# Performance work log

Hardware: AMD Instinct MI355X
Metric: run time of the kernel (lower is better)

## Reference

```python
import jax, jax.numpy as jnp
import numpy as np

B = 8192       # batch
HID = 1024     # hidden_dim
HEADS = 8      # head_count
OBS, ACT, N_AGENTS = 128, 32, 4
ENC_IN = N_AGENTS * OBS + ACT   # 544
DEC_IN = (N_AGENTS - 1) * ACT   # 96


def _linear(key, fan_in, fan_out):
    k1, k2 = jax.random.split(key)
    lim = 1.0 / np.sqrt(fan_in)
    W = jax.random.uniform(k1, (fan_in, fan_out), minval=-lim, maxval=lim, dtype=jnp.float32)
    b = jax.random.uniform(k2, (fan_out,), minval=-lim, maxval=lim, dtype=jnp.float32)
    return W, b


def setup_inputs() -> dict:
    key = jax.random.key(0)
    ks = jax.random.split(key, 10)
    s = jax.random.normal(ks[0], (B, N_AGENTS * OBS), dtype=jnp.float32)
    a = jax.random.normal(ks[1], (B, N_AGENTS * ACT), dtype=jnp.float32)
    W_enc_in, b_enc_in = _linear(ks[2], ENC_IN, HID)   # encoder_input_fc
    W_dec_in, b_dec_in = _linear(ks[3], DEC_IN, HID)   # decoder_input_fc
    W_eh, b_eh = _linear(ks[4], HID, HID)              # fc_encoder_input
    head_ks = jax.random.split(ks[5], HEADS)
    Wb = [_linear(k, HID, HID) for k in head_ks]       # fc_encoder_heads
    W_heads = jnp.stack([w for w, _ in Wb], axis=0)    # [H, HID, HID]
    b_heads = jnp.stack([b for _, b in Wb], axis=0)    # [H, HID]
    W_dh, b_dh = _linear(ks[6], HID, HID)              # fc_decoder_input
    W1, b1 = _linear(ks[7], HID, HID)                  # fc1
    W2, b2 = _linear(ks[8], HID, 1)                    # fc2
    return {"s": s, "a": a,
            "W_enc_in": W_enc_in, "b_enc_in": b_enc_in,
            "W_dec_in": W_dec_in, "b_dec_in": b_dec_in,
            "W_eh": W_eh, "b_eh": b_eh,
            "W_heads": W_heads, "b_heads": b_heads,
            "W_dh": W_dh, "b_dh": b_dh,
            "W1": W1, "b1": b1, "W2": W2, "b2": b2}


def reference(s, a, W_enc_in, b_enc_in, W_dec_in, b_dec_in, W_eh, b_eh,
              W_heads, b_heads, W_dh, b_dh, W1, b1, W2, b2):
    relu = jax.nn.relu
    # agent id = 0: own action is a[:, :ACT], others' actions are a[:, ACT:]
    enc_input = jnp.concatenate([s, a[:, :ACT]], axis=1) @ W_enc_in + b_enc_in   # [B, HID]
    dec_input = a[:, ACT:] @ W_dec_in + b_dec_in                                 # [B, HID]
    # Attention_ATT_2
    encoder_h = relu(enc_input @ W_eh + b_eh)                                    # [B, HID]
    encoder_heads = relu(jnp.einsum('bd,hde->hbe', encoder_h, W_heads)
                         + b_heads[:, None, :])                                  # [H, B, HID]
    decoder_H = relu(dec_input @ W_dh + b_dh)                                    # [B, HID]
    scores = jnp.einsum('hbd,bd->bh', encoder_heads, decoder_H)                  # [B, H]
    attn = jax.nn.softmax(scores, axis=1)                                        # [B, H]
    context = jnp.einsum('hbd,bh->bd', encoder_heads, attn)                      # [B, HID]
    x = relu(context @ W1 + b1)
    q = x @ W2 + b2                                                              # [B, 1]
    return q
```

## Files before the change

kernel.cpp:

```cpp
#include <hip/hip_runtime.h>
#include <hip/hip_bf16.h>
#include <hip/hip_fp16.h>

#define BATCH   8192
#define HID     1024
#define HEADS   8
#define BC      2048

typedef unsigned int  u32;
typedef unsigned short u16;
typedef __attribute__((ext_vector_type(8))) short bf16x8;
typedef __attribute__((ext_vector_type(4))) float f32x4;

__device__ __forceinline__ u32 pack_hi2(u32 u0, u32 u1) {
    return (u0 >> 16) | (u1 & 0xFFFF0000u);
}
__device__ __forceinline__ void split1(float x, u16& h, u16& l) {
    const u32 u = __float_as_uint(x);
    h = (u16)(u >> 16);
    const float r = x - __uint_as_float(u & 0xFFFF0000u);
    l = (u16)(__float_as_uint(r) >> 16);
}
__device__ __forceinline__ void splitA4(float4 v, uint2& hi, uint2& lo) {
    u32 u0 = __float_as_uint(v.x), u1 = __float_as_uint(v.y),
        u2 = __float_as_uint(v.z), u3 = __float_as_uint(v.w);
    float r0 = v.x - __uint_as_float(u0 & 0xFFFF0000u);
    float r1 = v.y - __uint_as_float(u1 & 0xFFFF0000u);
    float r2 = v.z - __uint_as_float(u2 & 0xFFFF0000u);
    float r3 = v.w - __uint_as_float(u3 & 0xFFFF0000u);
    hi.x = pack_hi2(u0, u1);
    hi.y = pack_hi2(u2, u3);
    lo.x = pack_hi2(__float_as_uint(r0), __float_as_uint(r1));
    lo.y = pack_hi2(__float_as_uint(r2), __float_as_uint(r3));
}

__device__ __forceinline__ void gld16(const u16* g, u16* l) {
    __builtin_amdgcn_global_load_lds(
        (const __attribute__((address_space(1))) u32*)g,
        (__attribute__((address_space(3))) u32*)l, 16, 0, 0);
}

struct WSplitArgs {
    const float* src[6];
    u16* hi[6];
    u16* lo[6];
};

__global__ __launch_bounds__(256) void split_weight_all(WSplitArgs args)
{
    const int z = blockIdx.z;
    int which, zz = 0;
    if (z < 3)       { which = z; }
    else if (z < 11) { which = 3; zz = z - 3; }
    else             { which = z - 7; }
    const int KT = (which == 4) ? 17 : (which == 5 ? 3 : 32);
    const int kt = blockIdx.x;
    if (kt >= KT) return;
    const int K = KT * 32;
    const long long zoff = (long long)zz * K * 1024;
    const float* W  = args.src[which] + zoff;
    u16* hi = args.hi[which] + zoff;
    u16* lo = args.lo[which] + zoff;

    const int n0  = blockIdx.y * 128;
    const int tid = threadIdx.x;
    const int k   = tid >> 3;
    const int ng  = (tid & 7) * 16;
    const float* src = W + (long long)(kt * 32 + k) * 1024 + n0 + ng;
    u16* dh = hi + ((long long)kt * 1024 + n0) * 32 + k;
    u16* dl = lo + ((long long)kt * 1024 + n0) * 32 + k;
#pragma unroll
    for (int t = 0; t < 4; t++) {
        const float4 v = *(const float4*)(src + t * 4);
        u16 h0, l0, h1, l1, h2, l2, h3, l3;
        split1(v.x, h0, l0); split1(v.y, h1, l1);
        split1(v.z, h2, l2); split1(v.w, h3, l3);
        const int nb = (ng + t * 4) * 32;
        dh[nb]      = h0; dl[nb]      = l0;
        dh[nb + 32] = h1; dl[nb + 32] = l1;
        dh[nb + 64] = h2; dl[nb + 64] = l2;
        dh[nb + 96] = h3; dl[nb + 96] = l3;
    }
}

#define PIPE_GEOM \
    const int tid  = threadIdx.x; \
    const int lane = tid & 63; \
    const int wv   = tid >> 6; \
    const int wm   = wv >> 1, wn = wv & 1; \
    const int fr   = lane & 15; \
    const int fq   = lane >> 4; \
    const int m0   = blockIdx.y * 256; \
    const int n0   = blockIdx.x * 128; \
    const int lro2 = (lane >> 2) * 32 + (((lane & 3) ^ ((lane >> 3) & 3)) * 8); \
    const int fqx2 = (fq ^ ((fr >> 1) & 3)) * 8; \
    const int wr   = wv * 16;

#define PSTAGE_HI(dst_, aoff_, boff_) { \
    u16* db_ = (dst_); \
    gld16(Ahp + (aoff_) + (long long)wr * 32 + lro2, db_ + wr * 32); \
    gld16(Ahp + (aoff_) + (long long)(128 + wr) * 32 + lro2, db_ + (128 + wr) * 32); \
    gld16(Bhp + (boff_) + (long long)wr * 32 + lro2, db_ + 16384 + wr * 32); }

#define PSTAGE_LO(dst_, aoff_, boff_) { \
    u16* db_ = (dst_); \
    gld16(Alp + (aoff_) + (long long)wr * 32 + lro2, db_ + 8192 + wr * 32); \
    gld16(Alp + (aoff_) + (long long)(128 + wr) * 32 + lro2, db_ + 8192 + (128 + wr) * 32); \
    gld16(Blp + (boff_) + (long long)wr * 32 + lro2, db_ + 20480 + wr * 32); }

#define PTILE(t_, STAGE0_, STAGE1_, TAILWAIT_) { \
    const u16* bufp = smem + ((t_) % 3) * 24576; \
    bf16x8 bh[4], bl[4], ah0[2], al0[2], ah1[2], al1[2]; \
    _Pragma("unroll") \
    for (int j = 0; j < 4; j++) { \
        const int off = (wn * 64 + j * 16 + fr) * 32 + fqx2; \
        bh[j] = *(const bf16x8*)(bufp + 16384 + off); \
        bl[j] = *(const bf16x8*)(bufp + 20480 + off); } \
    _Pragma("unroll") \
    for (int i = 0; i < 2; i++) { \
        const int off = (wm * 64 + i * 16 + fr) * 32 + fqx2; \
        ah0[i] = *(const bf16x8*)(bufp + off); \
        al0[i] = *(const bf16x8*)(bufp + 8192 + off); } \
    STAGE0_; \
    __builtin_amdgcn_s_barrier(); \
    __builtin_amdgcn_s_setprio(1); \
    _Pragma("unroll") \
    for (int i = 0; i < 2; i++) \
        _Pragma("unroll") \
        for (int j = 0; j < 4; j++) { \
            acc[i][j] = __builtin_amdgcn_mfma_f32_16x16x32_bf16(ah0[i], bh[j], acc[i][j], 0, 0, 0); \
            acc[i][j] = __builtin_amdgcn_mfma_f32_16x16x32_bf16(ah0[i], bl[j], acc[i][j], 0, 0, 0); \
            acc[i][j] = __builtin_amdgcn_mfma_f32_16x16x32_bf16(al0[i], bh[j], acc[i][j], 0, 0, 0); } \
    __builtin_amdgcn_s_setprio(0); \
    __builtin_amdgcn_s_barrier(); \
    __builtin_amdgcn_sched_barrier(0); \
    _Pragma("unroll") \
    for (int i = 0; i < 2; i++) { \
        const int off = (wm * 64 + (2 + i) * 16 + fr) * 32 + fqx2; \
        ah1[i] = *(const bf16x8*)(bufp + off); \
        al1[i] = *(const bf16x8*)(bufp + 8192 + off); } \
    STAGE1_; \
    __builtin_amdgcn_s_barrier(); \
    __builtin_amdgcn_s_setprio(1); \
    _Pragma("unroll") \
    for (int i = 0; i < 2; i++) \
        _Pragma("unroll") \
        for (int j = 0; j < 4; j++) { \
            acc[2 + i][j] = __builtin_amdgcn_mfma_f32_16x16x32_bf16(ah1[i], bh[j], acc[2 + i][j], 0, 0, 0); \
            acc[2 + i][j] = __builtin_amdgcn_mfma_f32_16x16x32_bf16(ah1[i], bl[j], acc[2 + i][j], 0, 0, 0); \
            acc[2 + i][j] = __builtin_amdgcn_mfma_f32_16x16x32_bf16(al1[i], bh[j], acc[2 + i][j], 0, 0, 0); } \
    __builtin_amdgcn_s_setprio(0); \
    TAILWAIT_; \
    __builtin_amdgcn_s_barrier(); \
    __builtin_amdgcn_sched_barrier(0); \
}

#define PIPE_LOOP \
    const int KT = K >> 5; \
    const long long astep = (long long)MA * 32; \
    const long long bstep = 32768; \
    const long long abase = ((long long)moff + m0) * 32; \
    const long long bbase = (long long)n0 * 32; \
    PSTAGE_HI(smem, abase, bbase); \
    PSTAGE_LO(smem, abase, bbase); \
    PSTAGE_HI(smem + 24576, abase + astep, bbase + bstep); \
    PSTAGE_LO(smem + 24576, abase + astep, bbase + bstep); \
    asm volatile("s_waitcnt vmcnt(6)" ::: "memory"); \
    __builtin_amdgcn_s_barrier(); \
    __builtin_amdgcn_sched_barrier(0); \
    for (int t = 0; t < KT - 2; t++) { \
        u16* dst2 = smem + ((t + 2) % 3) * 24576; \
        const long long a2 = abase + (long long)(t + 2) * astep; \
        const long long b2 = bbase + (long long)(t + 2) * bstep; \
        PTILE(t, PSTAGE_HI(dst2, a2, b2), PSTAGE_LO(dst2, a2, b2), \
              asm volatile("s_waitcnt vmcnt(6)" ::: "memory")); \
    } \
    PTILE(KT - 2, ((void)0), ((void)0), \
          asm volatile("s_waitcnt vmcnt(0)" ::: "memory")); \
    PTILE(KT - 1, ((void)0), ((void)0), ((void)0));

template <int RELU, int OUTP>
__global__ __launch_bounds__(512) void gemm_fast(
    const u16* __restrict__ Ahp, const u16* __restrict__ Alp, int MA, int moff,
    const u16* __restrict__ Bhp, const u16* __restrict__ Blp,
    const float* __restrict__ bias,
    float* __restrict__ Cf,
    u16* __restrict__ Chp, u16* __restrict__ Clp, int MC,
    int K)
{
    __shared__ alignas(16) u16 smem[3 * 24576];
    PIPE_GEOM

    f32x4 acc[4][4];
#pragma unroll
    for (int i = 0; i < 4; i++)
#pragma unroll
        for (int j = 0; j < 4; j++) acc[i][j] = 0;

    PIPE_LOOP

#pragma unroll
    for (int j = 0; j < 4; j++) {
        const int n = n0 + wn * 64 + j * 16 + fr;
        const float bb = bias[n];
#pragma unroll
        for (int i = 0; i < 4; i++) {
#pragma unroll
            for (int r = 0; r < 4; r++) {
                const int m = m0 + wm * 64 + i * 16 + fq * 4 + r;
                float v = acc[i][j][r] + bb;
                if (RELU) v = fmaxf(v, 0.0f);
                if (OUTP) {
                    u16 h, l;
                    split1(v, h, l);
                    const long long d = ((long long)(n >> 5) * MC + moff + m) * 32 + (n & 31);
                    Chp[d] = h;
                    Clp[d] = l;
                } else {
                    Cf[(long long)m * 1024 + n] = v;
                }
            }
        }
    }
}

__global__ __launch_bounds__(512) void heads_kernel(
    const u16* __restrict__ Ahp, const u16* __restrict__ Alp, int MA, int moff,
    const u16* __restrict__ Whp, const u16* __restrict__ Wlp,
    const float* __restrict__ b_heads,
    const float* __restrict__ decH,
    __half* __restrict__ headsb,
    float* __restrict__ scoresp)
{
    __shared__ alignas(16) u16 smem[3 * 24576];
    __shared__ float scred[2][256];
    PIPE_GEOM
    const int h = blockIdx.z;
    const u16* Bhp = Whp + (long long)h * 1048576;
    const u16* Blp = Wlp + (long long)h * 1048576;
    const float* bias = b_heads + h * 1024;
    const int K = 1024;

    f32x4 acc[4][4];
#pragma unroll
    for (int i = 0; i < 4; i++)
#pragma unroll
        for (int j = 0; j < 4; j++) acc[i][j] = 0;

    PIPE_LOOP

    float part[4][4];
#pragma unroll
    for (int i = 0; i < 4; i++)
#pragma unroll
        for (int r = 0; r < 4; r++) part[i][r] = 0.0f;

#pragma unroll
    for (int j = 0; j < 4; j++) {
        const int n = n0 + wn * 64 + j * 16 + fr;
        const float bb = bias[n];
#pragma unroll
        for (int i = 0; i < 4; i++) {
#pragma unroll
            for (int r = 0; r < 4; r++) {
                const int b_loc = m0 + wm * 64 + i * 16 + fq * 4 + r;
                const float v = fmaxf(acc[i][j][r] + bb, 0.0f);
                headsb[((long long)b_loc * HEADS + h) * 1024 + n] = __float2half(v);
                part[i][r] = fmaf(v, decH[(long long)b_loc * 1024 + n], part[i][r]);
            }
        }
    }
#pragma unroll
    for (int off = 1; off < 16; off <<= 1)
#pragma unroll
        for (int i = 0; i < 4; i++)
#pragma unroll
            for (int r = 0; r < 4; r++)
                part[i][r] += __shfl_xor(part[i][r], off, 64);

    if (fr == 0) {
#pragma unroll
        for (int i = 0; i < 4; i++)
#pragma unroll
            for (int r = 0; r < 4; r++)
                scred[wn][wm * 64 + i * 16 + fq * 4 + r] = part[i][r];
    }
    __syncthreads();
    if (tid < 256) {
        const float sv = scred[0][tid] + scred[1][tid];
        scoresp[(long long)(h * 8 + blockIdx.x) * BC + m0 + tid] = sv;
    }
}

template <int RELU>
__global__ __launch_bounds__(256) void gemm_cvt(
    const float* __restrict__ src1, int lda1, int kofs1,
    const float* __restrict__ src2, int lda2, int ksplit,
    const u16* __restrict__ Bhp, const u16* __restrict__ Blp,
    const float* __restrict__ bias,
    u16* __restrict__ Chp, u16* __restrict__ Clp, int MC,
    int K)
{
    __shared__ alignas(16) u16 Ah[4096], Al[4096], Bh[4096], Bl[4096];
    const int tid  = threadIdx.x;
    const int lane = tid & 63;
    const int wv   = tid >> 6;
    const int wm   = wv >> 1, wn = wv & 1;
    const int fr   = lane & 15;
    const int fq   = lane >> 4;
    const int m0   = blockIdx.y * 128;
    const int n0   = blockIdx.x * 128;
    const int fqx  = (fq ^ (fr & 3)) * 8;
    const int lro  = (lane >> 2) * 32 + (((lane & 3) ^ ((lane >> 2) & 3)) * 8);
    const int br0  = wv * 16;
    const int br1  = 64 + wv * 16;
    const int ar   = tid >> 3;
    const int akq  = tid & 7;
    const int awoff = (((akq >> 1) ^ (ar & 3)) * 8) + (akq & 1) * 4;

    f32x4 acc[4][4];
#pragma unroll
    for (int i = 0; i < 4; i++)
#pragma unroll
        for (int j = 0; j < 4; j++) acc[i][j] = 0;

    const int KT = K >> 5;
    for (int kt = 0; kt < KT; kt++) {
        const int k0 = kt * 32;
        const float* srcp; int ldk, kc;
        if (k0 < ksplit) { srcp = src1; ldk = lda1; kc = k0 + kofs1; }
        else             { srcp = src2; ldk = lda2; kc = k0 - ksplit; }

        const u16* Bg  = Bhp + ((long long)kt * 1024 + n0) * 32;
        const u16* Bg2 = Blp + ((long long)kt * 1024 + n0) * 32;
        gld16(Bg  + br0 * 32 + lro, &Bh[br0 * 32]);
        gld16(Bg  + br1 * 32 + lro, &Bh[br1 * 32]);
        gld16(Bg2 + br0 * 32 + lro, &Bl[br0 * 32]);
        gld16(Bg2 + br1 * 32 + lro, &Bl[br1 * 32]);

#pragma unroll
        for (int it = 0; it < 4; it++) {
            const int row = ar + it * 32;
            const float4 v = *(const float4*)(srcp + (long long)(m0 + row) * ldk + kc + akq * 4);
            uint2 hi, lo;
            splitA4(v, hi, lo);
            *(uint2*)&Ah[row * 32 + awoff] = hi;
            *(uint2*)&Al[row * 32 + awoff] = lo;
        }
        __syncthreads();

        bf16x8 ah[4], al[4], bh[4], bl[4];
#pragma unroll
        for (int i = 0; i < 4; i++) {
            const int off = (wm * 64 + i * 16 + fr) * 32 + fqx;
            ah[i] = *(const bf16x8*)&Ah[off];
            al[i] = *(const bf16x8*)&Al[off];
        }
#pragma unroll
        for (int j = 0; j < 4; j++) {
            const int off = (wn * 64 + j * 16 + fr) * 32 + fqx;
            bh[j] = *(const bf16x8*)&Bh[off];
            bl[j] = *(const bf16x8*)&Bl[off];
        }
#pragma unroll
        for (int i = 0; i < 4; i++)
#pragma unroll
            for (int j = 0; j < 4; j++) {
                acc[i][j] = __builtin_amdgcn_mfma_f32_16x16x32_bf16(ah[i], bh[j], acc[i][j], 0, 0, 0);
                acc[i][j] = __builtin_amdgcn_mfma_f32_16x16x32_bf16(ah[i], bl[j], acc[i][j], 0, 0, 0);
                acc[i][j] = __builtin_amdgcn_mfma_f32_16x16x32_bf16(al[i], bh[j], acc[i][j], 0, 0, 0);
            }
        __syncthreads();
    }

#pragma unroll
    for (int j = 0; j < 4; j++) {
        const int n = n0 + wn * 64 + j * 16 + fr;
        const float bb = bias[n];
#pragma unroll
        for (int i = 0; i < 4; i++) {
#pragma unroll
            for (int r = 0; r < 4; r++) {
                const int m = m0 + wm * 64 + i * 16 + fq * 4 + r;
                float v = acc[i][j][r] + bb;
                if (RELU) v = fmaxf(v, 0.0f);
                u16 h, l;
                split1(v, h, l);
                const long long d = ((long long)(n >> 5) * MC + m) * 32 + (n & 31);
                Chp[d] = h;
                Clp[d] = l;
            }
        }
    }
}

__global__ __launch_bounds__(256) void context_kernel(
    const __half* __restrict__ headsb, const float* __restrict__ scoresp,
    u16* __restrict__ ctx_hi, u16* __restrict__ ctx_lo, int MC, int row0)
{
    __shared__ float sc_s[64];
    __shared__ float attn_s[HEADS];
    const int b = blockIdx.x;
    const int tid = threadIdx.x;
    if (tid < 64) sc_s[tid] = scoresp[(long long)tid * BC + b];
    __syncthreads();
    if (tid == 0) {
        float sc[HEADS];
#pragma unroll
        for (int h = 0; h < HEADS; h++) {
            float s = 0.0f;
#pragma unroll
            for (int nt = 0; nt < 8; nt++) s += sc_s[h * 8 + nt];
            sc[h] = s;
        }
        float mx = sc[0];
#pragma unroll
        for (int h = 1; h < HEADS; h++) mx = fmaxf(mx, sc[h]);
        float e[HEADS], sum = 0.0f;
#pragma unroll
        for (int h = 0; h < HEADS; h++) { e[h] = __expf(sc[h] - mx); sum += e[h]; }
        const float inv = 1.0f / sum;
#pragma unroll
        for (int h = 0; h < HEADS; h++) attn_s[h] = e[h] * inv;
    }
    __syncthreads();

    const int d = tid * 4;
    float w[HEADS];
#pragma unroll
    for (int h = 0; h < HEADS; h++) w[h] = attn_s[h];
    float4 acc = make_float4(0.f, 0.f, 0.f, 0.f);
#pragma unroll
    for (int h = 0; h < HEADS; h++) {
        const __half2* hp = (const __half2*)(headsb + ((long long)b * HEADS + h) * 1024 + d);
        const float2 f0 = __half22float2(hp[0]);
        const float2 f1 = __half22float2(hp[1]);
        acc.x = fmaf(w[h], f0.x, acc.x);
        acc.y = fmaf(w[h], f0.y, acc.y);
        acc.z = fmaf(w[h], f1.x, acc.z);
        acc.w = fmaf(w[h], f1.y, acc.w);
    }
    uint2 hi, lo;
    splitA4(acc, hi, lo);
    const long long off = ((long long)(d >> 5) * MC + row0 + b) * 32 + (d & 31);
    *(uint2*)(ctx_hi + off) = hi;
    *(uint2*)(ctx_lo + off) = lo;
}

__global__ __launch_bounds__(256) void fc2_kernel(
    const float* __restrict__ x, const float* __restrict__ W2,
    const float* __restrict__ b2, float* __restrict__ q)
{
    const int b   = blockIdx.x;
    const int tid = threadIdx.x;
    __shared__ float red[4];

    const float4 xv = *(const float4*)(x + (long long)b * 1024 + tid * 4);
    const float4 wv = *(const float4*)(W2 + tid * 4);
    float p = xv.x * wv.x + xv.y * wv.y + xv.z * wv.z + xv.w * wv.w;
#pragma unroll
    for (int off = 32; off > 0; off >>= 1) p += __shfl_down(p, off, 64);
    if ((tid & 63) == 0) red[tid >> 6] = p;
    __syncthreads();
    if (tid == 0) q[b] = red[0] + red[1] + red[2] + red[3] + b2[0];
}

extern "C" void kernel_launch(void* const* d_in, const int* in_sizes, int n_in,
                              void* d_out, int out_size, void* d_ws, size_t ws_size,
                              hipStream_t stream)
{
    const float* s        = (const float*)d_in[0];
    const float* a        = (const float*)d_in[1];
    const float* W_enc_in = (const float*)d_in[2];
    const float* b_enc_in = (const float*)d_in[3];
    const float* W_dec_in = (const float*)d_in[4];
    const float* b_dec_in = (const float*)d_in[5];
    const float* W_eh     = (const float*)d_in[6];
    const float* b_eh     = (const float*)d_in[7];
    const float* W_heads  = (const float*)d_in[8];
    const float* b_heads  = (const float*)d_in[9];
    const float* W_dh     = (const float*)d_in[10];
    const float* b_dh     = (const float*)d_in[11];
    const float* W1       = (const float*)d_in[12];
    const float* b1       = (const float*)d_in[13];
    const float* W2       = (const float*)d_in[14];
    const float* b2       = (const float*)d_in[15];
    float* q_out = (float*)d_out;

    u16* P = (u16*)d_ws;
    u16* enc_hi = P; P += 557056;
    u16* enc_lo = P; P += 557056;
    u16* dec_hi = P; P += 98304;
    u16* dec_lo = P; P += 98304;
    u16* eh_hi  = P; P += 1048576;
    u16* eh_lo  = P; P += 1048576;
    u16* dh_hi  = P; P += 1048576;
    u16* dh_lo  = P; P += 1048576;
    u16* w1_hi  = P; P += 1048576;
    u16* w1_lo  = P; P += 1048576;
    u16* wh_hi  = P; P += 8388608;
    u16* wh_lo  = P; P += 8388608;
    char* act = (char*)P;

    const dim3 blk(256);
    const dim3 blk512(512);

    WSplitArgs wa;
    wa.src[0] = W_eh;    wa.hi[0] = eh_hi;  wa.lo[0] = eh_lo;
    wa.src[1] = W_dh;    wa.hi[1] = dh_hi;  wa.lo[1] = dh_lo;
    wa.src[2] = W1;      wa.hi[2] = w1_hi;  wa.lo[2] = w1_lo;
    wa.src[3] = W_heads; wa.hi[3] = wh_hi;  wa.lo[3] = wh_lo;
    wa.src[4] = W_enc_in; wa.hi[4] = enc_hi; wa.lo[4] = enc_lo;
    wa.src[5] = W_dec_in; wa.hi[5] = dec_hi; wa.lo[5] = dec_lo;
    split_weight_all<<<dim3(32, 8, 13), blk, 0, stream>>>(wa);

    const bool high = (ws_size >= 150011904ULL);

    if (high) {
        u16*    bufA_hi = (u16*)act;
        u16*    bufA_lo = bufA_hi + 8388608;
        __half* headsb  = (__half*)act;
        u16*    encH_hi = (u16*)(act + 33554432);
        u16*    encH_lo = encH_hi + 8388608;
        float*  decH    = (float*)(act + 2LL * 33554432);
        float*  scoresp = (float*)(act + 3LL * 33554432);

        const dim3 ggc(8, 64, 1);
        const dim3 ggf(8, 32, 1);
        gemm_cvt<0><<<ggc, blk, 0, stream>>>(s, 512, 0, a, 128, 512,
            enc_hi, enc_lo, b_enc_in, bufA_hi, bufA_lo, 8192, 544);
        gemm_fast<1, 1><<<ggf, blk512, 0, stream>>>(bufA_hi, bufA_lo, 8192, 0,
            eh_hi, eh_lo, b_eh, nullptr, encH_hi, encH_lo, 8192, 1024);
        gemm_cvt<0><<<ggc, blk, 0, stream>>>(a, 128, 32, a, 128, 1 << 28,
            dec_hi, dec_lo, b_dec_in, bufA_hi, bufA_lo, 8192, 96);
        gemm_fast<1, 0><<<ggf, blk512, 0, stream>>>(bufA_hi, bufA_lo, 8192, 0,
            dh_hi, dh_lo, b_dh, decH, nullptr, nullptr, 0, 1024);

        for (int c = 0; c < BATCH / BC; c++) {
            heads_kernel<<<dim3(8, BC / 256, 8), blk512, 0, stream>>>(
                encH_hi, encH_lo, 8192, c * BC, wh_hi, wh_lo, b_heads,
                decH + (long long)c * BC * 1024, headsb, scoresp);
            context_kernel<<<dim3(BC), blk, 0, stream>>>(
                headsb, scoresp, encH_hi, encH_lo, 8192, c * BC);
        }
        gemm_fast<1, 0><<<ggf, blk512, 0, stream>>>(encH_hi, encH_lo, 8192, 0,
            w1_hi, w1_lo, b1, decH, nullptr, nullptr, 0, 1024);
        fc2_kernel<<<dim3(BATCH), blk, 0, stream>>>(decH, W2, b2, q_out);
    } else {
        __half* headsb  = (__half*)act;
        u16*    bufA_hi = (u16*)act;
        u16*    bufA_lo = bufA_hi + 2097152;
        u16*    encH_hi = (u16*)(act + 33554432);
        u16*    encH_lo = encH_hi + 2097152;
        float*  decH    = (float*)(act + 33554432 + 8388608);
        float*  scoresp = (float*)(act + 33554432 + 2LL * 8388608);

        const dim3 ggc(8, BC / 128, 1);
        const dim3 ggf(8, BC / 256, 1);
        for (int c = 0; c < BATCH / BC; c++) {
            const float* sC = s + (long long)c * BC * 512;
            const float* aC = a + (long long)c * BC * 128;
            gemm_cvt<0><<<ggc, blk, 0, stream>>>(sC, 512, 0, aC, 128, 512,
                enc_hi, enc_lo, b_enc_in, bufA_hi, bufA_lo, BC, 544);
            gemm_fast<1, 1><<<ggf, blk512, 0, stream>>>(bufA_hi, bufA_lo, BC, 0,
                eh_hi, eh_lo, b_eh, nullptr, encH_hi, encH_lo, BC, 1024);
            gemm_cvt<0><<<ggc, blk, 0, stream>>>(aC, 128, 32, aC, 128, 1 << 28,
                dec_hi, dec_lo, b_dec_in, bufA_hi, bufA_lo, BC, 96);
            gemm_fast<1, 0><<<ggf, blk512, 0, stream>>>(bufA_hi, bufA_lo, BC, 0,
                dh_hi, dh_lo, b_dh, decH, nullptr, nullptr, 0, 1024);
            heads_kernel<<<dim3(8, BC / 256, 8), blk512, 0, stream>>>(
                encH_hi, encH_lo, BC, 0, wh_hi, wh_lo, b_heads,
                decH, headsb, scoresp);
            context_kernel<<<dim3(BC), blk, 0, stream>>>(
                headsb, scoresp, encH_hi, encH_lo, BC, 0);
            gemm_fast<1, 0><<<ggf, blk512, 0, stream>>>(encH_hi, encH_lo, BC, 0,
                w1_hi, w1_lo, b1, decH, nullptr, nullptr, 0, 1024);
            fc2_kernel<<<dim3(BC), blk, 0, stream>>>(decH, W2, b2, q_out + (long long)c * BC);
        }
    }
}
```

Measured before the change: 757.5 us.

## Load low-part bf16 fragments directly from global, halving LDS staging

The split-bf16 GEMM pipeline now stages only the high halves of A and B in LDS. The low halves are loaded straight from global memory into registers, one tile ahead, using a ping-pong register set. This halves shared memory per block (three buffers of 12288 elements) so launch_bounds can request two blocks per CU, raising occupancy. In exchange it adds register pressure and uncoalesced-ish direct global loads for the low parts, and reorders the MFMA schedule into three passes per tile.

```diff
diff --git a/kernel.cpp b/kernel.cpp
--- a/kernel.cpp
+++ b/kernel.cpp
@@ -96,91 +96,80 @@
     const int fqx2 = (fq ^ ((fr >> 1) & 3)) * 8; \
     const int wr   = wv * 16;
 
-#define PSTAGE_HI(dst_, aoff_, boff_) { \
-    u16* db_ = (dst_); \
-    gld16(Ahp + (aoff_) + (long long)wr * 32 + lro2, db_ + wr * 32); \
-    gld16(Ahp + (aoff_) + (long long)(128 + wr) * 32 + lro2, db_ + (128 + wr) * 32); \
-    gld16(Bhp + (boff_) + (long long)wr * 32 + lro2, db_ + 16384 + wr * 32); }
-
-#define PSTAGE_LO(dst_, aoff_, boff_) { \
-    u16* db_ = (dst_); \
-    gld16(Alp + (aoff_) + (long long)wr * 32 + lro2, db_ + 8192 + wr * 32); \
-    gld16(Alp + (aoff_) + (long long)(128 + wr) * 32 + lro2, db_ + 8192 + (128 + wr) * 32); \
-    gld16(Blp + (boff_) + (long long)wr * 32 + lro2, db_ + 20480 + wr * 32); }
-
-#define PTILE(t_, STAGE0_, STAGE1_, TAILWAIT_) { \
-    const u16* bufp = smem + ((t_) % 3) * 24576; \
-    bf16x8 bh[4], bl[4], ah0[2], al0[2], ah1[2], al1[2]; \
+#define PSTAGE(bi_, t_) { \
+    u16* db_ = smem + (bi_) * 12288; \
+    const long long ao_ = abase + (long long)(t_) * astep; \
+    const long long bo_ = bbase + (long long)(t_) * 32768; \
+    gld16(Ahp + ao_ + (long long)wr * 32 + lro2, db_ + wr * 32); \
+    gld16(Ahp + ao_ + (long long)(128 + wr) * 32 + lro2, db_ + (128 + wr) * 32); \
+    gld16(Bhp + bo_ + (long long)wr * 32 + lro2, db_ + 8192 + wr * 32); }
+
+#define PLO(la_, lb_, t_) { \
+    const long long ao_ = abase + (long long)(t_) * astep; \
+    const long long bo_ = bbase + (long long)(t_) * 32768; \
     _Pragma("unroll") \
-    for (int j = 0; j < 4; j++) { \
-        const int off = (wn * 64 + j * 16 + fr) * 32 + fqx2; \
-        bh[j] = *(const bf16x8*)(bufp + 16384 + off); \
-        bl[j] = *(const bf16x8*)(bufp + 20480 + off); } \
+    for (int i_ = 0; i_ < 4; i_++) { \
+        la_[i_] = *(const bf16x8*)(Alp + ao_ + (long long)(wm * 64 + i_ * 16 + fr) * 32 + fq * 8); \
+        lb_[i_] = *(const bf16x8*)(Blp + bo_ + (long long)(wn * 64 + i_ * 16 + fr) * 32 + fq * 8); } }
+
+#define PFRAGS(bi_) \
+    const u16* bufp_ = smem + (bi_) * 12288; \
+    bf16x8 ah[4], bh[4]; \
     _Pragma("unroll") \
-    for (int i = 0; i < 2; i++) { \
-        const int off = (wm * 64 + i * 16 + fr) * 32 + fqx2; \
-        ah0[i] = *(const bf16x8*)(bufp + off); \
-        al0[i] = *(const bf16x8*)(bufp + 8192 + off); } \
-    STAGE0_; \
-    __builtin_amdgcn_s_barrier(); \
+    for (int i_ = 0; i_ < 4; i_++) \
+        ah[i_] = *(const bf16x8*)(bufp_ + (wm * 64 + i_ * 16 + fr) * 32 + fqx2); \
+    _Pragma("unroll") \
+    for (int j_ = 0; j_ < 4; j_++) \
+        bh[j_] = *(const bf16x8*)(bufp_ + 8192 + (wn * 64 + j_ * 16 + fr) * 32 + fqx2);
+
+#define PMFMA(la_, lb_) \
+    __builtin_amdgcn_sched_barrier(0); \
     __builtin_amdgcn_s_setprio(1); \
     _Pragma("unroll") \
-    for (int i = 0; i < 2; i++) \
+    for (int i_ = 0; i_ < 4; i_++) \
         _Pragma("unroll") \
-        for (int j = 0; j < 4; j++) { \
-            acc[i][j] = __builtin_amdgcn_mfma_f32_16x16x32_bf16(ah0[i], bh[j], acc[i][j], 0, 0, 0); \
-            acc[i][j] = __builtin_amdgcn_mfma_f32_16x16x32_bf16(ah0[i], bl[j], acc[i][j], 0, 0, 0); \
-            acc[i][j] = __builtin_amdgcn_mfma_f32_16x16x32_bf16(al0[i], bh[j], acc[i][j], 0, 0, 0); } \
-    __builtin_amdgcn_s_setprio(0); \
+        for (int j_ = 0; j_ < 4; j_++) \
+            acc[i_][j_] = __builtin_amdgcn_mfma_f32_16x16x32_bf16(ah[i_], bh[j_], acc[i_][j_], 0, 0, 0); \
+    _Pragma("unroll") \
+    for (int i_ = 0; i_ < 4; i_++) \
+        _Pragma("unroll") \
+        for (int j_ = 0; j_ < 4; j_++) \
+            acc[i_][j_] = __builtin_amdgcn_mfma_f32_16x16x32_bf16(ah[i_], lb_[j_], acc[i_][j_], 0, 0, 0); \
+    _Pragma("unroll") \
+    for (int i_ = 0; i_ < 4; i_++) \
+        _Pragma("unroll") \
+        for (int j_ = 0; j_ < 4; j_++) \
+            acc[i_][j_] = __builtin_amdgcn_mfma_f32_16x16x32_bf16(la_[i_], bh[j_], acc[i_][j_], 0, 0, 0); \
+    __builtin_amdgcn_s_setprio(0);
+
+#define PBAR(W_) \
+    asm volatile("s_waitcnt vmcnt(" #W_ ")" ::: "memory"); \
     __builtin_amdgcn_s_barrier(); \
-    __builtin_amdgcn_sched_barrier(0); \
-    _Pragma("unroll") \
-    for (int i = 0; i < 2; i++) { \
-        const int off = (wm * 64 + (2 + i) * 16 + fr) * 32 + fqx2; \
-        ah1[i] = *(const bf16x8*)(bufp + off); \
-        al1[i] = *(const bf16x8*)(bufp + 8192 + off); } \
-    STAGE1_; \
-    __builtin_amdgcn_s_barrier(); \
-    __builtin_amdgcn_s_setprio(1); \
-    _Pragma("unroll") \
-    for (int i = 0; i < 2; i++) \
-        _Pragma("unroll") \
-        for (int j = 0; j < 4; j++) { \
-            acc[2 + i][j] = __builtin_amdgcn_mfma_f32_16x16x32_bf16(ah1[i], bh[j], acc[2 + i][j], 0, 0, 0); \
-            acc[2 + i][j] = __builtin_amdgcn_mfma_f32_16x16x32_bf16(ah1[i], bl[j], acc[2 + i][j], 0, 0, 0); \
-            acc[2 + i][j] = __builtin_amdgcn_mfma_f32_16x16x32_bf16(al1[i], bh[j], acc[2 + i][j], 0, 0, 0); } \
-    __builtin_amdgcn_s_setprio(0); \
-    TAILWAIT_; \
-    __builtin_amdgcn_s_barrier(); \
-    __builtin_amdgcn_sched_barrier(0); \
-}
+    __builtin_amdgcn_sched_barrier(0);
 
 #define PIPE_LOOP \
     const int KT = K >> 5; \
     const long long astep = (long long)MA * 32; \
-    const long long bstep = 32768; \
     const long long abase = ((long long)moff + m0) * 32; \
     const long long bbase = (long long)n0 * 32; \
-    PSTAGE_HI(smem, abase, bbase); \
-    PSTAGE_LO(smem, abase, bbase); \
-    PSTAGE_HI(smem + 24576, abase + astep, bbase + bstep); \
-    PSTAGE_LO(smem + 24576, abase + astep, bbase + bstep); \
-    asm volatile("s_waitcnt vmcnt(6)" ::: "memory"); \
-    __builtin_amdgcn_s_barrier(); \
-    __builtin_amdgcn_sched_barrier(0); \
-    for (int t = 0; t < KT - 2; t++) { \
-        u16* dst2 = smem + ((t + 2) % 3) * 24576; \
-        const long long a2 = abase + (long long)(t + 2) * astep; \
-        const long long b2 = bbase + (long long)(t + 2) * bstep; \
-        PTILE(t, PSTAGE_HI(dst2, a2, b2), PSTAGE_LO(dst2, a2, b2), \
-              asm volatile("s_waitcnt vmcnt(6)" ::: "memory")); \
+    bf16x8 loAa[4], loAb[4], loBa[4], loBb[4]; \
+    PSTAGE(0, 0); \
+    PSTAGE(1, 1); \
+    PLO(loAa, loAb, 0); \
+    PBAR(11) \
+    int be = 0, bo = 1, bs = 2; \
+    for (int t = 0; t + 2 < KT; t += 2) { \
+        { PFRAGS(be) PSTAGE(bs, t + 2); PLO(loBa, loBb, t + 1); \
+          PMFMA(loAa, loAb) PBAR(11) } \
+        { PFRAGS(bo) PSTAGE(be, t + 3); PLO(loAa, loAb, t + 2); \
+          PMFMA(loBa, loBb) PBAR(11) } \
+        const int nb_ = bs; bs = bo; bo = be; be = nb_; \
     } \
-    PTILE(KT - 2, ((void)0), ((void)0), \
-          asm volatile("s_waitcnt vmcnt(0)" ::: "memory")); \
-    PTILE(KT - 1, ((void)0), ((void)0), ((void)0));
+    { PFRAGS(be) PLO(loBa, loBb, KT - 1); PMFMA(loAa, loAb) PBAR(8) } \
+    { PFRAGS(bo) PMFMA(loBa, loBb) }
 
 template <int RELU, int OUTP>
-__global__ __launch_bounds__(512) void gemm_fast(
+__global__ __launch_bounds__(512, 2) void gemm_fast(
     const u16* __restrict__ Ahp, const u16* __restrict__ Alp, int MA, int moff,
     const u16* __restrict__ Bhp, const u16* __restrict__ Blp,
     const float* __restrict__ bias,
@@ -188,7 +177,7 @@
     u16* __restrict__ Chp, u16* __restrict__ Clp, int MC,
     int K)
 {
-    __shared__ alignas(16) u16 smem[3 * 24576];
+    __shared__ alignas(16) u16 smem[3 * 12288];
     PIPE_GEOM
 
     f32x4 acc[4][4];
@@ -224,7 +213,7 @@
     }
 }
 
-__global__ __launch_bounds__(512) void heads_kernel(
+__global__ __launch_bounds__(512, 2) void heads_kernel(
     const u16* __restrict__ Ahp, const u16* __restrict__ Alp, int MA, int moff,
     const u16* __restrict__ Whp, const u16* __restrict__ Wlp,
     const float* __restrict__ b_heads,
@@ -232,7 +221,7 @@
     __half* __restrict__ headsb,
     float* __restrict__ scoresp)
 {
-    __shared__ alignas(16) u16 smem[3 * 24576];
+    __shared__ alignas(16) u16 smem[3 * 12288];
     __shared__ float scred[2][256];
     PIPE_GEOM
     const int h = blockIdx.z;
```

Measured after the change: 808.5 us. 1.07x slower.
